# Performance work log

Hardware: AMD Instinct MI355X
Metric: run time of the kernel (lower is better)

The kernel has to match this reference:

```python
import jax, jax.numpy as jnp
import numpy as np

OUT, IN, G = 12288, 4096, 128       # out_features, in_features, group_size
IN_GROUPS = IN // G                 # 32
QMAX = 15                           # wbit=4


def setup_inputs() -> dict:
    key = jax.random.key(0)
    k1, k2, k3, k4, k5 = jax.random.split(key, 5)
    x = jax.random.normal(k1, (8, IN), dtype=jnp.float32)
    # packed 4-bit codes: two nibbles per byte, high nibble first
    qcodes = jax.random.randint(k2, (OUT, IN_GROUPS, G // 2), 0, 256, dtype=jnp.int32).astype(jnp.uint8)
    scales = jax.random.uniform(k3, (OUT, IN_GROUPS), dtype=jnp.float32, minval=0.005, maxval=0.02)
    zeros = jax.random.uniform(k4, (OUT, IN_GROUPS), dtype=jnp.float32, minval=0.0, maxval=float(QMAX))
    bias = jax.random.normal(k5, (OUT,), dtype=jnp.float32) * 0.01
    return {"x": x, "qcodes": qcodes, "scales": scales, "zeros": zeros, "bias": bias}


def _dequant_weight(qcodes, scales, zeros):
    # unpack nibbles: q[0::2] = high nibble, q[1::2] = low nibble (matches torch packing)
    hi = (qcodes >> 4) & 0xF                     # [OUT, IN_GROUPS, G//2]
    lo = qcodes & 0xF
    q = jnp.stack([hi, lo], axis=-1).reshape(OUT, IN_GROUPS, G).astype(jnp.float32)
    W = (q - zeros[..., None]) * scales[..., None]   # per-group affine dequant
    # torch reference casts to fp16 and slices to in_features
    return W.reshape(OUT, IN_GROUPS * G)[:, :IN].astype(jnp.float16)


def reference(x, qcodes, scales, zeros, bias):
    W = _dequant_weight(qcodes, scales, zeros)   # [OUT, IN] fp16
    return x @ W.astype(x.dtype).T + bias        # F.linear(x, W, bias)
```

## Files before the change

kernel.cpp:

```cpp
#include <hip/hip_runtime.h>
#include <cstdint>

#define OUTF 12288
#define INF  4096
#define NG   32
#define BATCH 8

#define BLOCK 512
#define WAVES 8
#define RPW 3
#define RPB (WAVES*RPW)
#define NBLK (OUTF/RPB)

typedef _Float16 half2_t __attribute__((ext_vector_type(2)));

__device__ __forceinline__ float dot2(half2_t a, half2_t b, float c) {
#if __has_builtin(__builtin_amdgcn_fdot2)
    return __builtin_amdgcn_fdot2(a, b, c, false);
#else
    return c + (float)(a.x) * (float)(b.x) + (float)(a.y) * (float)(b.y);
#endif
}

__device__ __forceinline__ half2_t pk16(float a, float b) {
    return __builtin_bit_cast(half2_t, __builtin_amdgcn_cvt_pkrtz(a, b));
}

__global__ __launch_bounds__(BLOCK, 4) void qlin_kernel(
    const float* __restrict__ x,
    const int*   __restrict__ qc,
    const float* __restrict__ scales,
    const float* __restrict__ zeros,
    const float* __restrict__ bias,
    float* __restrict__ out)
{
    __shared__ uint4 xs[4096];

    const int tid  = threadIdx.x;
    const int wave = tid >> 6;
    const int lane = tid & 63;
    const int row0 = blockIdx.x * RPB + wave * RPW;

    #pragma unroll
    for (int i = 0; i < 8; ++i) {
        const float4 v0 = *reinterpret_cast<const float4*>(x + i * INF + tid * 8);
        const float4 v1 = *reinterpret_cast<const float4*>(x + i * INF + tid * 8 + 4);
        uint4 w;
        w.x = __builtin_bit_cast(uint32_t, pk16(v0.x, v0.y));
        w.y = __builtin_bit_cast(uint32_t, pk16(v0.z, v0.w));
        w.z = __builtin_bit_cast(uint32_t, pk16(v1.x, v1.y));
        w.w = __builtin_bit_cast(uint32_t, pk16(v1.z, v1.w));
        xs[i * 512 + tid] = w;
    }

    const int* qp[RPW];
    const float* scb[RPW];
    const float* zpb[RPW];
    #pragma unroll
    for (int r = 0; r < RPW; ++r) {
        const int o = row0 + r;
        qp[r]  = qc + o * 2048 + lane * 4;
        scb[r] = scales + o * NG + (lane >> 4);
        zpb[r] = zeros  + o * NG + (lane >> 4);
    }

    uint4 tA[RPW], tB[RPW];
    float sA[RPW], nzA[RPW], sB[RPW], nzB[RPW];
    #pragma unroll
    for (int r = 0; r < RPW; ++r) {
        tA[r]  = *reinterpret_cast<const uint4*>(qp[r]);
        tB[r]  = *reinterpret_cast<const uint4*>(qp[r] + 256);
        sA[r]  = scb[r][0];
        nzA[r] = -zpb[r][0] * sA[r];
    }

    float y[RPW][BATCH];
    #pragma unroll
    for (int r = 0; r < RPW; ++r)
        #pragma unroll
        for (int b = 0; b < BATCH; ++b) y[r][b] = 0.f;

    __syncthreads();

    #pragma unroll
    for (int h = 0; h < 8; ++h) {
        uint4 tN[RPW];
        if (h < 6) {
            #pragma unroll
            for (int r = 0; r < RPW; ++r)
                tN[r] = *reinterpret_cast<const uint4*>(qp[r] + (h + 2) * 256);
        }
        if (h < 7) {
            #pragma unroll
            for (int r = 0; r < RPW; ++r) {
                sB[r]  = scb[r][(h + 1) * 4];
                nzB[r] = -zpb[r][(h + 1) * 4] * sB[r];
            }
        }

        half2_t wp[RPW][4];
        #pragma unroll
        for (int r = 0; r < RPW; ++r) {
            #pragma unroll
            for (int e = 0; e < 4; ++e) {
                const uint32_t ei = (e == 0) ? tA[r].x : (e == 1) ? tA[r].y
                                 : (e == 2) ? tA[r].z : tA[r].w;
                const float hi = (float)((ei >> 4) & 0xFu);
                const float lo = (float)( ei       & 0xFu);
                wp[r][e] = pk16(fmaf(hi, sA[r], nzA[r]),
                                fmaf(lo, sA[r], nzA[r]));
            }
        }

        const int slot = h * 64 + lane;
        #pragma unroll
        for (int b = 0; b < BATCH; ++b) {
            const uint4 v = xs[b * 512 + slot];
            const half2_t x0 = __builtin_bit_cast(half2_t, v.x);
            const half2_t x1 = __builtin_bit_cast(half2_t, v.y);
            const half2_t x2 = __builtin_bit_cast(half2_t, v.z);
            const half2_t x3 = __builtin_bit_cast(half2_t, v.w);
            #pragma unroll
            for (int r = 0; r < RPW; ++r) {
                y[r][b] = dot2(wp[r][0], x0, y[r][b]);
                y[r][b] = dot2(wp[r][1], x1, y[r][b]);
                y[r][b] = dot2(wp[r][2], x2, y[r][b]);
                y[r][b] = dot2(wp[r][3], x3, y[r][b]);
            }
        }

        #pragma unroll
        for (int r = 0; r < RPW; ++r) {
            tA[r] = tB[r];
            if (h < 6) tB[r] = tN[r];
            if (h < 7) { sA[r] = sB[r]; nzA[r] = nzB[r]; }
        }
    }

    float keep = 0.f;
    #pragma unroll
    for (int r = 0; r < RPW; ++r) {
        #pragma unroll
        for (int b = 0; b < BATCH; ++b) {
            float v = y[r][b];
            #pragma unroll
            for (int m = 1; m < 64; m <<= 1) v += __shfl_xor(v, m, 64);
            if (lane == r * 8 + b) keep = v;
        }
    }
    if (lane < RPW * BATCH) {
        const int r = lane >> 3, b = lane & 7;
        const int o = row0 + r;
        out[b * OUTF + o] = keep + bias[o];
    }
}

extern "C" void kernel_launch(void* const* d_in, const int* in_sizes, int n_in,
                              void* d_out, int out_size, void* d_ws, size_t ws_size,
                              hipStream_t stream) {
    const float* x      = (const float*)d_in[0];
    const int*   qcodes = (const int*)  d_in[1];
    const float* scales = (const float*)d_in[2];
    const float* zeros  = (const float*)d_in[3];
    const float* bias   = (const float*)d_in[4];
    float* out = (float*)d_out;

    qlin_kernel<<<NBLK, BLOCK, 0, stream>>>(x, qcodes, scales, zeros, bias, out);
}
```

Measured before the change: 27.56 us.

## Process rows sequentially with 32-byte per-lane weight loads and triple buffering

```diff
diff --git a/kernel.cpp b/kernel.cpp
--- a/kernel.cpp
+++ b/kernel.cpp
@@ -21,7 +21,6 @@
     return c + (float)(a.x) * (float)(b.x) + (float)(a.y) * (float)(b.y);
 #endif
 }
-
 __device__ __forceinline__ half2_t pk16(float a, float b) {
     return __builtin_bit_cast(half2_t, __builtin_amdgcn_cvt_pkrtz(a, b));
 }
@@ -41,6 +40,14 @@
     const int lane = tid & 63;
     const int row0 = blockIdx.x * RPB + wave * RPW;
 
+    const int* qbase = qc + row0 * 2048 + lane * 8;
+
+    uint4 qb[3][2];
+    qb[0][0] = *reinterpret_cast<const uint4*>(qbase + 0);
+    qb[0][1] = *reinterpret_cast<const uint4*>(qbase + 4);
+    qb[1][0] = *reinterpret_cast<const uint4*>(qbase + 512);
+    qb[1][1] = *reinterpret_cast<const uint4*>(qbase + 516);
+
     #pragma unroll
     for (int i = 0; i < 8; ++i) {
         const float4 v0 = *reinterpret_cast<const float4*>(x + i * INF + tid * 8);
@@ -53,25 +60,16 @@
         xs[i * 512 + tid] = w;
     }
 
-    const int* qp[RPW];
-    const float* scb[RPW];
-    const float* zpb[RPW];
+    float sc_[RPW][4], nz_[RPW][4];
     #pragma unroll
     for (int r = 0; r < RPW; ++r) {
-        const int o = row0 + r;
-        qp[r]  = qc + o * 2048 + lane * 4;
-        scb[r] = scales + o * NG + (lane >> 4);
-        zpb[r] = zeros  + o * NG + (lane >> 4);
-    }
-
-    uint4 tA[RPW], tB[RPW];
-    float sA[RPW], nzA[RPW], sB[RPW], nzB[RPW];
-    #pragma unroll
-    for (int r = 0; r < RPW; ++r) {
-        tA[r]  = *reinterpret_cast<const uint4*>(qp[r]);
-        tB[r]  = *reinterpret_cast<const uint4*>(qp[r] + 256);
-        sA[r]  = scb[r][0];
-        nzA[r] = -zpb[r][0] * sA[r];
+        #pragma unroll
+        for (int cc = 0; cc < 4; ++cc) {
+            const int a = (row0 + r) * NG + cc * 8 + (lane >> 3);
+            const float s = scales[a];
+            sc_[r][cc] = s;
+            nz_[r][cc] = -zeros[a] * s;
+        }
     }
 
     float y[RPW][BATCH];
@@ -83,57 +81,46 @@
     __syncthreads();
 
     #pragma unroll
-    for (int h = 0; h < 8; ++h) {
-        uint4 tN[RPW];
-        if (h < 6) {
-            #pragma unroll
-            for (int r = 0; r < RPW; ++r)
-                tN[r] = *reinterpret_cast<const uint4*>(qp[r] + (h + 2) * 256);
-        }
-        if (h < 7) {
-            #pragma unroll
-            for (int r = 0; r < RPW; ++r) {
-                sB[r]  = scb[r][(h + 1) * 4];
-                nzB[r] = -zpb[r][(h + 1) * 4] * sB[r];
-            }
+    for (int c = 0; c < 12; ++c) {
+        const int r  = c >> 2;
+        const int cc = c & 3;
+
+        if (c < 10) {
+            const int c2  = c + 2;
+            const int off = (c2 >> 2) * 2048 + (c2 & 3) * 512;
+            qb[c2 % 3][0] = *reinterpret_cast<const uint4*>(qbase + off);
+            qb[c2 % 3][1] = *reinterpret_cast<const uint4*>(qbase + off + 4);
         }
 
-        half2_t wp[RPW][4];
-        #pragma unroll
-        for (int r = 0; r < RPW; ++r) {
+        const uint4 t0 = qb[c % 3][0];
+        const uint4 t1 = qb[c % 3][1];
+        const float s_ = sc_[r][cc];
+        const float n_ = nz_[r][cc];
+
+        half2_t wp[8];
+        {
+            const uint32_t e[8] = {t0.x, t0.y, t0.z, t0.w, t1.x, t1.y, t1.z, t1.w};
             #pragma unroll
-            for (int e = 0; e < 4; ++e) {
-                const uint32_t ei = (e == 0) ? tA[r].x : (e == 1) ? tA[r].y
-                                 : (e == 2) ? tA[r].z : tA[r].w;
-                const float hi = (float)((ei >> 4) & 0xFu);
-                const float lo = (float)( ei       & 0xFu);
-                wp[r][e] = pk16(fmaf(hi, sA[r], nzA[r]),
-                                fmaf(lo, sA[r], nzA[r]));
-            }
+            for (int i = 0; i < 8; ++i)
+                wp[i] = pk16(fmaf((float)((e[i] >> 4) & 0xFu), s_, n_),
+                             fmaf((float)( e[i]       & 0xFu), s_, n_));
         }
 
-        const int slot = h * 64 + lane;
+        const int sbase = cc * 128 + lane * 2;
         #pragma unroll
         for (int b = 0; b < BATCH; ++b) {
-            const uint4 v = xs[b * 512 + slot];
-            const half2_t x0 = __builtin_bit_cast(half2_t, v.x);
-            const half2_t x1 = __builtin_bit_cast(half2_t, v.y);
-            const half2_t x2 = __builtin_bit_cast(half2_t, v.z);
-            const half2_t x3 = __builtin_bit_cast(half2_t, v.w);
-            #pragma unroll
-            for (int r = 0; r < RPW; ++r) {
-                y[r][b] = dot2(wp[r][0], x0, y[r][b]);
-                y[r][b] = dot2(wp[r][1], x1, y[r][b]);
-                y[r][b] = dot2(wp[r][2], x2, y[r][b]);
-                y[r][b] = dot2(wp[r][3], x3, y[r][b]);
-            }
-        }
-
-        #pragma unroll
-        for (int r = 0; r < RPW; ++r) {
-            tA[r] = tB[r];
-            if (h < 6) tB[r] = tN[r];
-            if (h < 7) { sA[r] = sB[r]; nzA[r] = nzB[r]; }
+            const uint4 v0 = xs[b * 512 + sbase];
+            const uint4 v1 = xs[b * 512 + sbase + 1];
+            float acc = y[r][b];
+            acc = dot2(wp[0], __builtin_bit_cast(half2_t, v0.x), acc);
+            acc = dot2(wp[1], __builtin_bit_cast(half2_t, v0.y), acc);
+            acc = dot2(wp[2], __builtin_bit_cast(half2_t, v0.z), acc);
+            acc = dot2(wp[3], __builtin_bit_cast(half2_t, v0.w), acc);
+            acc = dot2(wp[4], __builtin_bit_cast(half2_t, v1.x), acc);
+            acc = dot2(wp[5], __builtin_bit_cast(half2_t, v1.y), acc);
+            acc = dot2(wp[6], __builtin_bit_cast(half2_t, v1.z), acc);
+            acc = dot2(wp[7], __builtin_bit_cast(half2_t, v1.w), acc);
+            y[r][b] = acc;
         }
     }
 
```

After: 45.15 us. 63.8% more time.
